# Performance work log

Measured on AMD Instinct MI355X. Metric: run time of the kernel, lower is better.

Reference implementation:

```python
import jax, jax.numpy as jnp
import numpy as np


def setup_inputs() -> dict:
    key = jax.random.key(0)
    # Head output: [batch, grid_h, grid_w, anchors, 5] = (x, y, w, h, score)
    # scores ~ U[0,1] so ~half the boxes pass the 0.5 threshold.
    X = jax.random.uniform(key, (128, 64, 64, 9, 5), dtype=jnp.float32)
    score_threshold = jnp.ones((1,), dtype=jnp.float32) * 0.5
    return {"X": X, "score_threshold": score_threshold}


def reference(X, score_threshold):
    # Faithful jax version of: reshape(-1,5); keep boxes with score>thr;
    # convert xywh -> xyxy. The torch code does a Python loop + stack
    # (variable-length compaction); in jax we compute the keep-mask and
    # the converted coords for all boxes, zeroing dropped ones, and
    # return the mask so downstream compaction is a prefix-sum away.
    boxes = X.reshape(-1, 5)                       # [N, 5]
    keep = boxes[:, 4] > score_threshold[0]        # [N] bool
    xy = boxes[:, 0:2]                             # centers
    half_wh = boxes[:, 2:4] * 0.5
    xyxy = jnp.concatenate([xy - half_wh, xy + half_wh], axis=-1)  # [N, 4]
    out = jnp.where(keep[:, None], xyxy, jnp.zeros((), dtype=xyxy.dtype))
    return out, keep
```

## Files before the change

kernel.cpp:

```cpp
#include <hip/hip_runtime.h>


using f4 = __attribute__((ext_vector_type(4))) float;

__global__ __launch_bounds__(256) void plate_kernel(
    const float* __restrict__ X,
    const float* __restrict__ thr_p,
    float* __restrict__ out_xyxy,
    float* __restrict__ out_keep,
    int ntiles)
{
    __shared__ float lds[5120];

    const int tile = blockIdx.x;
    if (tile >= ntiles) return;
    const int j = threadIdx.x;
    const float thr = thr_p[0];

    const f4* __restrict__ src = reinterpret_cast<const f4*>(X) + (size_t)tile * 1280;
    f4* __restrict__ ldsv = reinterpret_cast<f4*>(lds);
    #pragma unroll
    for (int k = 0; k < 5; ++k)
        ldsv[k * 256 + j] = src[k * 256 + j];

    __syncthreads();

    f4*    __restrict__ dst = reinterpret_cast<f4*>(out_xyxy) + (size_t)tile * 1024;
    float* __restrict__ kp  = out_keep + (size_t)tile * 1024;

    #pragma unroll
    for (int k = 0; k < 4; ++k) {
        const int m = k * 256 + j;
        const float x = lds[5 * m + 0];
        const float y = lds[5 * m + 1];
        const float w = lds[5 * m + 2];
        const float h = lds[5 * m + 3];
        const float s = lds[5 * m + 4];
        const bool keep = s > thr;
        const float hw = w * 0.5f;
        const float hh = h * 0.5f;
        f4 r;
        r.x = keep ? (x - hw) : 0.0f;
        r.y = keep ? (y - hh) : 0.0f;
        r.z = keep ? (x + hw) : 0.0f;
        r.w = keep ? (y + hh) : 0.0f;
        __builtin_nontemporal_store(r, &dst[m]);
        __builtin_nontemporal_store(keep ? 1.0f : 0.0f, &kp[m]);
    }
}

extern "C" void kernel_launch(void* const* d_in, const int* in_sizes, int n_in,
                              void* d_out, int out_size, void* d_ws, size_t ws_size,
                              hipStream_t stream)
{
    const float* X   = (const float*)d_in[0];
    const float* thr = (const float*)d_in[1];

    const long long n_boxes = (long long)in_sizes[0] / 5;
    const int ntiles = (int)(n_boxes / 1024);

    float* out_xyxy = (float*)d_out;
    float* out_keep = (float*)d_out + n_boxes * 4;

    plate_kernel<<<ntiles, 256, 0, stream>>>(X, thr, out_xyxy, out_keep, ntiles);
}
```

Measured before the change: 32.75 us.

## Stage tiles with direct global-to-LDS loads and double-buffer two tiles per block

Each block now handles two consecutive 1024-box tiles. Input is copied straight into LDS with `global_load_lds`, which skips the register round trip. The second tile's load is issued before the first tile is computed and stored, so load latency overlaps the store phase. In exchange, LDS per block doubles, which may lower occupancy. The kernel also now relies on the tile count being even, since the bounds check was dropped.

```diff
diff --git a/kernel.cpp b/kernel.cpp
--- a/kernel.cpp
+++ b/kernel.cpp
@@ -3,50 +3,72 @@
 
 using f4 = __attribute__((ext_vector_type(4))) float;
 
+typedef __attribute__((address_space(1))) const void gconst;
+typedef __attribute__((address_space(3))) void svoid;
+
 __global__ __launch_bounds__(256) void plate_kernel(
     const float* __restrict__ X,
     const float* __restrict__ thr_p,
     float* __restrict__ out_xyxy,
-    float* __restrict__ out_keep,
-    int ntiles)
+    float* __restrict__ out_keep)
 {
-    __shared__ float lds[5120];
+    __shared__ float lds[2][5120];
 
-    const int tile = blockIdx.x;
-    if (tile >= ntiles) return;
+    const int b = blockIdx.x;
     const int j = threadIdx.x;
+    const int wbase = j & ~63;
     const float thr = thr_p[0];
 
-    const f4* __restrict__ src = reinterpret_cast<const f4*>(X) + (size_t)tile * 1280;
-    f4* __restrict__ ldsv = reinterpret_cast<f4*>(lds);
-    #pragma unroll
-    for (int k = 0; k < 5; ++k)
-        ldsv[k * 256 + j] = src[k * 256 + j];
+    const int t0 = 2 * b;
+    const int t1 = 2 * b + 1;
 
+    #define STAGE(buf, tile)                                                     \
+        {                                                                        \
+            const float* gsrc = X + (size_t)(tile) * 5120;                       \
+            _Pragma("unroll")                                                    \
+            for (int k = 0; k < 5; ++k) {                                        \
+                __builtin_amdgcn_global_load_lds(                                \
+                    (gconst*)(gsrc + 4 * (k * 256 + j)),                         \
+                    (svoid*)&lds[buf][4 * (k * 256 + wbase)],                    \
+                    16, 0, 0);                                                   \
+            }                                                                    \
+        }
+
+    #define COMPUTE(buf, tile)                                                   \
+        {                                                                        \
+            f4*    __restrict__ dst = reinterpret_cast<f4*>(out_xyxy)            \
+                                      + (size_t)(tile) * 1024;                   \
+            float* __restrict__ kp  = out_keep + (size_t)(tile) * 1024;          \
+            _Pragma("unroll")                                                    \
+            for (int k = 0; k < 4; ++k) {                                        \
+                const int m = k * 256 + j;                                       \
+                const float x = lds[buf][5 * m + 0];                             \
+                const float y = lds[buf][5 * m + 1];                             \
+                const float w = lds[buf][5 * m + 2];                             \
+                const float h = lds[buf][5 * m + 3];                             \
+                const float s = lds[buf][5 * m + 4];                             \
+                const bool keep = s > thr;                                       \
+                const float hw = w * 0.5f;                                       \
+                const float hh = h * 0.5f;                                       \
+                f4 r;                                                            \
+                r.x = keep ? (x - hw) : 0.0f;                                    \
+                r.y = keep ? (y - hh) : 0.0f;                                    \
+                r.z = keep ? (x + hw) : 0.0f;                                    \
+                r.w = keep ? (y + hh) : 0.0f;                                    \
+                __builtin_nontemporal_store(r, &dst[m]);                         \
+                __builtin_nontemporal_store(keep ? 1.0f : 0.0f, &kp[m]);         \
+            }                                                                    \
+        }
+
+    STAGE(0, t0);
     __syncthreads();
+    STAGE(1, t1);
+    COMPUTE(0, t0);
+    __syncthreads();
+    COMPUTE(1, t1);
 
-    f4*    __restrict__ dst = reinterpret_cast<f4*>(out_xyxy) + (size_t)tile * 1024;
-    float* __restrict__ kp  = out_keep + (size_t)tile * 1024;
-
-    #pragma unroll
-    for (int k = 0; k < 4; ++k) {
-        const int m = k * 256 + j;
-        const float x = lds[5 * m + 0];
-        const float y = lds[5 * m + 1];
-        const float w = lds[5 * m + 2];
-        const float h = lds[5 * m + 3];
-        const float s = lds[5 * m + 4];
-        const bool keep = s > thr;
-        const float hw = w * 0.5f;
-        const float hh = h * 0.5f;
-        f4 r;
-        r.x = keep ? (x - hw) : 0.0f;
-        r.y = keep ? (y - hh) : 0.0f;
-        r.z = keep ? (x + hw) : 0.0f;
-        r.w = keep ? (y + hh) : 0.0f;
-        __builtin_nontemporal_store(r, &dst[m]);
-        __builtin_nontemporal_store(keep ? 1.0f : 0.0f, &kp[m]);
-    }
+    #undef STAGE
+    #undef COMPUTE
 }
 
 extern "C" void kernel_launch(void* const* d_in, const int* in_sizes, int n_in,
@@ -58,9 +80,10 @@
 
     const long long n_boxes = (long long)in_sizes[0] / 5;
     const int ntiles = (int)(n_boxes / 1024);
+    const int npairs = ntiles / 2;
 
     float* out_xyxy = (float*)d_out;
     float* out_keep = (float*)d_out + n_boxes * 4;
 
-    plate_kernel<<<ntiles, 256, 0, stream>>>(X, thr, out_xyxy, out_keep, ntiles);
+    plate_kernel<<<npairs, 256, 0, stream>>>(X, thr, out_xyxy, out_keep);
 }
```

New measurement: 32.73 us. Within noise of the previous version (-0.1%).
